# Optimization experiments

Measured on AMD Instinct MI355X. Metric: run time of the kernel, lower is better.

The kernel has to match this reference:

```python
import jax, jax.numpy as jnp
import numpy as np

B, NUM, LENTH, AUX = 32, 64, 64, 64
SIZE, OUT = 256, 256
IN_G = (LENTH + 1) * 2 + AUX  # 194


def _linear_params(k, fan_in, fan_out):
    # torch nn.Linear default init: U(-1/sqrt(fan_in), 1/sqrt(fan_in))
    s = 1.0 / np.sqrt(fan_in)
    kw, kb = jax.random.split(k)
    W = jax.random.uniform(kw, (fan_in, fan_out), minval=-s, maxval=s, dtype=jnp.float32)
    b = jax.random.uniform(kb, (fan_out,), minval=-s, maxval=s, dtype=jnp.float32)
    return W, b


def setup_inputs() -> dict:
    key = jax.random.key(0)
    ks = jax.random.split(key, 8)
    inp = {"x_aux": jax.random.normal(ks[0], (B, NUM, LENTH + AUX), dtype=jnp.float32)}
    dims = [("g1", IN_G, SIZE), ("g2", SIZE, SIZE), ("g3", SIZE, SIZE), ("g4", SIZE, OUT),
            ("f1", OUT, SIZE), ("f2", SIZE, SIZE), ("f3", SIZE, OUT)]
    for k, (name, fi, fo) in zip(ks[1:], dims):
        W, b = _linear_params(k, fi, fo)
        inp[name + "_w"] = W
        inp[name + "_b"] = b
    return inp


def reference(x_aux, g1_w, g1_b, g2_w, g2_b, g3_w, g3_b, g4_w, g4_b,
              f1_w, f1_b, f2_w, f2_b, f3_w, f3_b):
    bsz = x_aux.shape[0]
    # coord feature = object index i
    coord = jnp.broadcast_to(
        jnp.arange(NUM, dtype=x_aux.dtype)[None, :, None], (bsz, NUM, 1))
    x = jnp.concatenate([x_aux[:, :, :LENTH], coord], axis=-1)      # [B, N, LENTH+1]
    xa = jnp.concatenate([x_aux, coord], axis=-1)                   # [B, N, LENTH+AUX+1]
    # all-pairs broadcast+concat -> [B, N, N, IN_G]
    x_i = jnp.broadcast_to(x[:, None, :, :], (bsz, NUM, NUM, LENTH + 1))
    x_j = jnp.broadcast_to(xa[:, :, None, :], (bsz, NUM, NUM, LENTH + AUX + 1))
    pairs = jnp.concatenate([x_i, x_j], axis=-1)
    # shared g-MLP over every pair
    h = jax.nn.relu(pairs @ g1_w + g1_b)
    h = jax.nn.relu(h @ g2_w + g2_b)
    h = jax.nn.relu(h @ g3_w + g3_b)
    h = jax.nn.relu(h @ g4_w + g4_b)
    # sum-pool over all N*N pairs -> [B, OUT]
    x_g = h.sum(axis=(1, 2))
    # f-MLP (dropout treated as identity / eval mode)
    x_f = jax.nn.relu(x_g @ f1_w + f1_b)
    x_f = jax.nn.relu(x_f @ f2_w + f2_b)
    return x_f @ f3_w + f3_b
```

## Files before the change

### kernel.cpp

```cpp
#include <hip/hip_runtime.h>

#define BATCH 32
#define NOBJ  64
#define PADK  264

typedef _Float16 f16x2 __attribute__((ext_vector_type(2)));
typedef _Float16 f16x4 __attribute__((ext_vector_type(4)));
typedef _Float16 f16x8 __attribute__((ext_vector_type(8)));
typedef float    f32x4 __attribute__((ext_vector_type(4)));
typedef float    f32x16 __attribute__((ext_vector_type(16)));

#define MFMA32(a, b, c) __builtin_amdgcn_mfma_f32_32x32x16_f16((a), (b), (c), 0, 0, 0)


__global__ __launch_bounds__(256) void precompute_ci(
    const float* __restrict__ x_aux, const float* __restrict__ g1w,
    float* __restrict__ ci) {
  __shared__ float xs[4][128];
  const int blk = blockIdx.x;
  const int b  = blk >> 4;
  const int i0 = (blk & 15) * 4;
  const int t  = threadIdx.x;

#pragma unroll
  for (int u = 0; u < 2; ++u) {
    int idx = u * 256 + t;
    int j = idx >> 7, k = idx & 127;
    xs[j][k] = x_aux[((size_t)(b * NOBJ + i0 + j)) * 128 + k];
  }
  __syncthreads();

  float c0 = 0.f, c1 = 0.f, c2 = 0.f, c3 = 0.f;
#pragma unroll 8
  for (int k = 0; k < 128; ++k) {
    float w = g1w[(size_t)(65 + k) * 256 + t];
    c0 += xs[0][k] * w; c1 += xs[1][k] * w;
    c2 += xs[2][k] * w; c3 += xs[3][k] * w;
  }
  float wc = g1w[(size_t)193 * 256 + t];
  c0 += (float)(i0 + 0) * wc;
  c1 += (float)(i0 + 1) * wc;
  c2 += (float)(i0 + 2) * wc;
  c3 += (float)(i0 + 3) * wc;
  ci[((size_t)(b * NOBJ + i0 + 0)) * 256 + t] = c0;
  ci[((size_t)(b * NOBJ + i0 + 1)) * 256 + t] = c1;
  ci[((size_t)(b * NOBJ + i0 + 2)) * 256 + t] = c2;
  ci[((size_t)(b * NOBJ + i0 + 3)) * 256 + t] = c3;
}

__global__ __launch_bounds__(256) void prep_weights(
    const float* __restrict__ g1w, const float* __restrict__ g2w,
    const float* __restrict__ g3w, const float* __restrict__ g4w,
    _Float16* __restrict__ wtf, float* __restrict__ xg) {
  __shared__ _Float16 tile[256][33];
  const int blk = blockIdx.x;
  const int t = threadIdx.x;
  xg[blk * 256 + t] = 0.0f;

  const int l  = blk >> 3;
  const int nt = blk & 7;
  const float* src = (l == 0) ? g1w : (l == 1) ? g2w : (l == 2) ? g3w : g4w;

  const int nn = t & 31, kb = t >> 5;
#pragma unroll 4
  for (int pass = 0; pass < 32; ++pass) {
    int kp = pass * 8 + kb;
    int kl;
    if (l == 0) {
      kl = (kp <= 64) ? kp : -1;
    } else {
      kl = 64 * (kp >> 6) + 32 * (kp & 1) + ((kp & 63) >> 1);
    }
    float v = (kl >= 0) ? src[(size_t)kl * 256 + nt * 32 + nn] : 0.0f;
    tile[kp][nn] = (_Float16)v;
  }
  __syncthreads();

  const int lane = t & 63;
  const int nfrag = lane & 31;
  const int kbase = (lane >> 5) * 8;
  _Float16* dst = wtf + ((size_t)(l * 8 + nt) * 16) * 512;
#pragma unroll
  for (int q = 0; q < 4; ++q) {
    int kk = (t >> 6) + 4 * q;
    f16x8 fr;
#pragma unroll
    for (int j = 0; j < 8; ++j)
      fr[j] = tile[kk * 16 + kbase + j][nfrag];
    *(f16x8*)(dst + (size_t)kk * 512 + lane * 8) = fr;
  }
}

template <int STEPS>
__device__ __forceinline__ void do_layer(
    const _Float16* __restrict__ bp0, const _Float16* __restrict__ bp1,
    const _Float16* __restrict__ arow, f32x16 acc[8]) {
  f16x8 b0[STEPS], b1[STEPS];
#pragma unroll
  for (int kk = 0; kk < STEPS; ++kk) {
    b0[kk] = *(const f16x8*)(bp0 + kk * 512);
    b1[kk] = *(const f16x8*)(bp1 + kk * 512);
  }
#pragma unroll
  for (int kk = 0; kk < STEPS; ++kk) {
#pragma unroll
    for (int m = 0; m < 4; ++m) {
      f16x8 a = *(const f16x8*)(arow + (size_t)m * 32 * PADK + kk * 16);
      acc[m * 2]     = MFMA32(a, b0[kk], acc[m * 2]);
      acc[m * 2 + 1] = MFMA32(a, b1[kk], acc[m * 2 + 1]);
    }
  }
}

__global__ __launch_bounds__(256, 2) void g_mlp_pool(
    const float* __restrict__ x_aux,
    const _Float16* __restrict__ wtf,
    const float* __restrict__ ci,
    const float* __restrict__ g1b, const float* __restrict__ g2b,
    const float* __restrict__ g3b, const float* __restrict__ g4b,
    float* __restrict__ xg) {
  __shared__ _Float16 As[128][PADK];

  const int b  = blockIdx.x >> 5;
  const int i0 = (blockIdx.x & 31) * 2;
  const int t  = threadIdx.x;

  {
    const float* xb = x_aux + (size_t)b * NOBJ * 128;
    const int c4 = t & 15, r0 = t >> 4;
#pragma unroll
    for (int it = 0; it < 8; ++it) {
      int r = it * 16 + r0;
      f32x4 v = *(const f32x4*)(xb + (size_t)(r & 63) * 128 + c4 * 4);
      f16x4 hh = {(_Float16)v[0], (_Float16)v[1], (_Float16)v[2], (_Float16)v[3]};
      *(f16x4*)&As[r][c4 * 4] = hh;
    }
    if (t < 128) {
      f16x8 z1 = {};
      z1[0] = (_Float16)(t & 63);
      *(f16x8*)&As[t][64] = z1;
      f16x8 z = {};
      *(f16x8*)&As[t][72] = z;
    }
  }
  __syncthreads();

  const int lane = t & 63;
  const int nq   = t >> 6;
  const int c31  = lane & 31;
  const int h    = lane >> 5;
  const int n0   = nq * 64;
  const float* gb[4] = {g1b, g2b, g3b, g4b};

  const float* cb = ci + (size_t)(b * NOBJ + i0) * 256;
  const float ci_v[2][2] = {{cb[n0 + c31], cb[n0 + 32 + c31]},
                            {cb[256 + n0 + c31], cb[256 + 32 + n0 + c31]}};

  for (int layer = 0; layer < 4; ++layer) {
    const float bv0 = gb[layer][n0 + c31];
    const float bv1 = gb[layer][n0 + 32 + c31];

    f32x16 acc[8];

    const _Float16* bp0 =
        wtf + ((size_t)(layer * 8 + nq * 2) * 16) * 512 + lane * 8;
    const _Float16* bp1 = bp0 + 16 * 512;
    const _Float16* arow = &As[c31][h * 8];

    if (layer == 0) {
#pragma unroll
      for (int m = 0; m < 4; ++m)
#pragma unroll
        for (int ns = 0; ns < 2; ++ns)
#pragma unroll
          for (int reg = 0; reg < 16; ++reg)
            acc[m * 2 + ns][reg] = ci_v[m >> 1][ns];
      do_layer<5>(bp0, bp1, arow, acc);
    } else {
#pragma unroll
      for (int x = 0; x < 8; ++x) acc[x] = (f32x16){};
      do_layer<16>(bp0, bp1, arow, acc);
    }

    if (layer < 3) {
      __syncthreads();
#pragma unroll
      for (int m = 0; m < 4; ++m)
#pragma unroll
        for (int g = 0; g < 4; ++g)
#pragma unroll
          for (int r = 0; r < 4; ++r) {
            const int row = m * 32 + g * 8 + h * 4 + r;
            const int reg = g * 4 + r;
            f16x2 pk = {(_Float16)fmaxf(acc[m * 2][reg] + bv0, 0.f),
                        (_Float16)fmaxf(acc[m * 2 + 1][reg] + bv1, 0.f)};
            *(f16x2*)&As[row][n0 + 2 * c31] = pk;
          }
      __syncthreads();
    } else {
      float s0 = 0.f, s1 = 0.f;
#pragma unroll
      for (int m = 0; m < 4; ++m)
#pragma unroll
        for (int reg = 0; reg < 16; ++reg) {
          s0 += fmaxf(acc[m * 2][reg] + bv0, 0.f);
          s1 += fmaxf(acc[m * 2 + 1][reg] + bv1, 0.f);
        }
      s0 += __shfl_xor(s0, 32, 64);
      s1 += __shfl_xor(s1, 32, 64);
      if (h == 0) {
        atomicAdd(&xg[b * 256 + n0 + c31], s0);
        atomicAdd(&xg[b * 256 + n0 + 32 + c31], s1);
      }
    }
  }
}

__global__ __launch_bounds__(1024) void f_mlp(
    const float* __restrict__ xg,
    const float* __restrict__ f1w, const float* __restrict__ f1b,
    const float* __restrict__ f2w, const float* __restrict__ f2b,
    const float* __restrict__ f3w, const float* __restrict__ f3b,
    float* __restrict__ out) {
  __shared__ float xs[256], ys[256], ps[4][256];
  const int b = blockIdx.x;
  const int t = threadIdx.x;
  const int n = t & 255;
  const int kc = t >> 8;

  if (t < 256) xs[t] = xg[b * 256 + t];
  __syncthreads();

  float p = 0.f;
#pragma unroll 8
  for (int k0 = 0; k0 < 64; ++k0) {
    int k = kc * 64 + k0;
    p += xs[k] * f1w[k * 256 + n];
  }
  ps[kc][n] = p;
  __syncthreads();
  if (t < 256)
    ys[t] = fmaxf(f1b[t] + ps[0][t] + ps[1][t] + ps[2][t] + ps[3][t], 0.f);
  __syncthreads();

  p = 0.f;
#pragma unroll 8
  for (int k0 = 0; k0 < 64; ++k0) {
    int k = kc * 64 + k0;
    p += ys[k] * f2w[k * 256 + n];
  }
  ps[kc][n] = p;
  __syncthreads();
  if (t < 256)
    xs[t] = fmaxf(f2b[t] + ps[0][t] + ps[1][t] + ps[2][t] + ps[3][t], 0.f);
  __syncthreads();

  p = 0.f;
#pragma unroll 8
  for (int k0 = 0; k0 < 64; ++k0) {
    int k = kc * 64 + k0;
    p += xs[k] * f3w[k * 256 + n];
  }
  ps[kc][n] = p;
  __syncthreads();
  if (t < 256)
    out[b * 256 + t] = f3b[t] + ps[0][t] + ps[1][t] + ps[2][t] + ps[3][t];
}

extern "C" void kernel_launch(void* const* d_in, const int* in_sizes, int n_in,
                              void* d_out, int out_size, void* d_ws, size_t ws_size,
                              hipStream_t stream) {
  const float* x_aux = (const float*)d_in[0];
  const float* g1w = (const float*)d_in[1];
  const float* g1b = (const float*)d_in[2];
  const float* g2w = (const float*)d_in[3];
  const float* g2b = (const float*)d_in[4];
  const float* g3w = (const float*)d_in[5];
  const float* g3b = (const float*)d_in[6];
  const float* g4w = (const float*)d_in[7];
  const float* g4b = (const float*)d_in[8];
  const float* f1w = (const float*)d_in[9];
  const float* f1b = (const float*)d_in[10];
  const float* f2w = (const float*)d_in[11];
  const float* f2b = (const float*)d_in[12];
  const float* f3w = (const float*)d_in[13];
  const float* f3b = (const float*)d_in[14];
  float* out = (float*)d_out;

  _Float16* wtf = (_Float16*)d_ws;
  float* xg = (float*)((char*)d_ws + 512u * 1024u);
  float* ci = (float*)((char*)d_ws + 512u * 1024u + 32u * 1024u);

  hipLaunchKernelGGL(precompute_ci, dim3(512), dim3(256), 0, stream,
                     x_aux, g1w, ci);
  hipLaunchKernelGGL(prep_weights, dim3(32), dim3(256), 0, stream,
                     g1w, g2w, g3w, g4w, wtf, xg);
  hipLaunchKernelGGL(g_mlp_pool, dim3(BATCH * 32), dim3(256), 0, stream,
                     x_aux, wtf, ci, g1b, g2b, g3b, g4b, xg);
  hipLaunchKernelGGL(f_mlp, dim3(BATCH), dim3(1024), 0, stream,
                     xg, f1w, f1b, f2w, f2b, f3w, f3b, out);
}
```

Baseline: 163.3 us.

## Merge prep kernels and fuse f-MLP into g-MLP tail via last-block counter

Combines the ci precompute and weight prep into one launch, and removes the separate f_mlp kernel by having the last block per batch (detected with an atomic counter) run the f-MLP. This cuts two kernel launches and their inter-kernel gaps. In exchange, the f-MLP now runs on 256 threads with a full 256-long serial dot product per thread, and correctness depends on fences and the counter being reset every call.

```diff
diff --git a/kernel.cpp b/kernel.cpp
--- a/kernel.cpp
+++ b/kernel.cpp
@@ -13,81 +13,82 @@
 #define MFMA32(a, b, c) __builtin_amdgcn_mfma_f32_32x32x16_f16((a), (b), (c), 0, 0, 0)
 
 
-__global__ __launch_bounds__(256) void precompute_ci(
-    const float* __restrict__ x_aux, const float* __restrict__ g1w,
-    float* __restrict__ ci) {
-  __shared__ float xs[4][128];
-  const int blk = blockIdx.x;
-  const int b  = blk >> 4;
-  const int i0 = (blk & 15) * 4;
-  const int t  = threadIdx.x;
-
-#pragma unroll
-  for (int u = 0; u < 2; ++u) {
-    int idx = u * 256 + t;
-    int j = idx >> 7, k = idx & 127;
-    xs[j][k] = x_aux[((size_t)(b * NOBJ + i0 + j)) * 128 + k];
-  }
-  __syncthreads();
-
-  float c0 = 0.f, c1 = 0.f, c2 = 0.f, c3 = 0.f;
-#pragma unroll 8
-  for (int k = 0; k < 128; ++k) {
-    float w = g1w[(size_t)(65 + k) * 256 + t];
-    c0 += xs[0][k] * w; c1 += xs[1][k] * w;
-    c2 += xs[2][k] * w; c3 += xs[3][k] * w;
-  }
-  float wc = g1w[(size_t)193 * 256 + t];
-  c0 += (float)(i0 + 0) * wc;
-  c1 += (float)(i0 + 1) * wc;
-  c2 += (float)(i0 + 2) * wc;
-  c3 += (float)(i0 + 3) * wc;
-  ci[((size_t)(b * NOBJ + i0 + 0)) * 256 + t] = c0;
-  ci[((size_t)(b * NOBJ + i0 + 1)) * 256 + t] = c1;
-  ci[((size_t)(b * NOBJ + i0 + 2)) * 256 + t] = c2;
-  ci[((size_t)(b * NOBJ + i0 + 3)) * 256 + t] = c3;
-}
-
-__global__ __launch_bounds__(256) void prep_weights(
+__global__ __launch_bounds__(256) void prep_all(
+    const float* __restrict__ x_aux,
     const float* __restrict__ g1w, const float* __restrict__ g2w,
     const float* __restrict__ g3w, const float* __restrict__ g4w,
-    _Float16* __restrict__ wtf, float* __restrict__ xg) {
+    _Float16* __restrict__ wtf, float* __restrict__ xg,
+    float* __restrict__ ci, int* __restrict__ cnt) {
   __shared__ _Float16 tile[256][33];
   const int blk = blockIdx.x;
   const int t = threadIdx.x;
-  xg[blk * 256 + t] = 0.0f;
-
-  const int l  = blk >> 3;
-  const int nt = blk & 7;
-  const float* src = (l == 0) ? g1w : (l == 1) ? g2w : (l == 2) ? g3w : g4w;
-
-  const int nn = t & 31, kb = t >> 5;
+
+  if (blk < 32) {
+    xg[blk * 256 + t] = 0.0f;
+    if (blk == 0 && t < 32) cnt[t] = 0;
+
+    const int l  = blk >> 3;
+    const int nt = blk & 7;
+    const float* src = (l == 0) ? g1w : (l == 1) ? g2w : (l == 2) ? g3w : g4w;
+
+    const int nn = t & 31, kb = t >> 5;
 #pragma unroll 4
-  for (int pass = 0; pass < 32; ++pass) {
-    int kp = pass * 8 + kb;
-    int kl;
-    if (l == 0) {
-      kl = (kp <= 64) ? kp : -1;
-    } else {
-      kl = 64 * (kp >> 6) + 32 * (kp & 1) + ((kp & 63) >> 1);
-    }
-    float v = (kl >= 0) ? src[(size_t)kl * 256 + nt * 32 + nn] : 0.0f;
-    tile[kp][nn] = (_Float16)v;
-  }
-  __syncthreads();
-
-  const int lane = t & 63;
-  const int nfrag = lane & 31;
-  const int kbase = (lane >> 5) * 8;
-  _Float16* dst = wtf + ((size_t)(l * 8 + nt) * 16) * 512;
-#pragma unroll
-  for (int q = 0; q < 4; ++q) {
-    int kk = (t >> 6) + 4 * q;
-    f16x8 fr;
-#pragma unroll
-    for (int j = 0; j < 8; ++j)
-      fr[j] = tile[kk * 16 + kbase + j][nfrag];
-    *(f16x8*)(dst + (size_t)kk * 512 + lane * 8) = fr;
+    for (int pass = 0; pass < 32; ++pass) {
+      int kp = pass * 8 + kb;
+      int kl;
+      if (l == 0) {
+        kl = (kp <= 64) ? kp : -1;
+      } else {
+        kl = 64 * (kp >> 6) + 32 * (kp & 1) + ((kp & 63) >> 1);
+      }
+      float v = (kl >= 0) ? src[(size_t)kl * 256 + nt * 32 + nn] : 0.0f;
+      tile[kp][nn] = (_Float16)v;
+    }
+    __syncthreads();
+
+    const int lane = t & 63;
+    const int nfrag = lane & 31;
+    const int kbase = (lane >> 5) * 8;
+    _Float16* dst = wtf + ((size_t)(l * 8 + nt) * 16) * 512;
+#pragma unroll
+    for (int q = 0; q < 4; ++q) {
+      int kk = (t >> 6) + 4 * q;
+      f16x8 fr;
+#pragma unroll
+      for (int j = 0; j < 8; ++j)
+        fr[j] = tile[kk * 16 + kbase + j][nfrag];
+      *(f16x8*)(dst + (size_t)kk * 512 + lane * 8) = fr;
+    }
+  } else {
+    float* xs = (float*)&tile[0][0];
+    const int blkc = blk - 32;
+    const int b  = blkc >> 4;
+    const int i0 = (blkc & 15) * 4;
+
+#pragma unroll
+    for (int u = 0; u < 2; ++u) {
+      int idx = u * 256 + t;
+      int j = idx >> 7, k = idx & 127;
+      xs[j * 128 + k] = x_aux[((size_t)(b * NOBJ + i0 + j)) * 128 + k];
+    }
+    __syncthreads();
+
+    float c0 = 0.f, c1 = 0.f, c2 = 0.f, c3 = 0.f;
+#pragma unroll 8
+    for (int k = 0; k < 128; ++k) {
+      float w = g1w[(size_t)(65 + k) * 256 + t];
+      c0 += xs[k] * w;       c1 += xs[128 + k] * w;
+      c2 += xs[256 + k] * w; c3 += xs[384 + k] * w;
+    }
+    float wc = g1w[(size_t)193 * 256 + t];
+    c0 += (float)(i0 + 0) * wc;
+    c1 += (float)(i0 + 1) * wc;
+    c2 += (float)(i0 + 2) * wc;
+    c3 += (float)(i0 + 3) * wc;
+    ci[((size_t)(b * NOBJ + i0 + 0)) * 256 + t] = c0;
+    ci[((size_t)(b * NOBJ + i0 + 1)) * 256 + t] = c1;
+    ci[((size_t)(b * NOBJ + i0 + 2)) * 256 + t] = c2;
+    ci[((size_t)(b * NOBJ + i0 + 3)) * 256 + t] = c3;
   }
 }
 
@@ -118,8 +119,14 @@
     const float* __restrict__ ci,
     const float* __restrict__ g1b, const float* __restrict__ g2b,
     const float* __restrict__ g3b, const float* __restrict__ g4b,
-    float* __restrict__ xg) {
+    float* __restrict__ xg,
+    int* __restrict__ cnt,
+    const float* __restrict__ f1w, const float* __restrict__ f1b,
+    const float* __restrict__ f2w, const float* __restrict__ f2b,
+    const float* __restrict__ f3w, const float* __restrict__ f3b,
+    float* __restrict__ out) {
   __shared__ _Float16 As[128][PADK];
+  __shared__ int is_last;
 
   const int b  = blockIdx.x >> 5;
   const int i0 = (blockIdx.x & 31) * 2;
@@ -154,7 +161,7 @@
 
   const float* cb = ci + (size_t)(b * NOBJ + i0) * 256;
   const float ci_v[2][2] = {{cb[n0 + c31], cb[n0 + 32 + c31]},
-                            {cb[256 + n0 + c31], cb[256 + 32 + n0 + c31]}};
+                            {cb[256 + n0 + c31], cb[256 + n0 + 32 + c31]}};
 
   for (int layer = 0; layer < 4; ++layer) {
     const float bv0 = gb[layer][n0 + c31];
@@ -214,57 +221,39 @@
       }
     }
   }
-}
-
-__global__ __launch_bounds__(1024) void f_mlp(
-    const float* __restrict__ xg,
-    const float* __restrict__ f1w, const float* __restrict__ f1b,
-    const float* __restrict__ f2w, const float* __restrict__ f2b,
-    const float* __restrict__ f3w, const float* __restrict__ f3b,
-    float* __restrict__ out) {
-  __shared__ float xs[256], ys[256], ps[4][256];
-  const int b = blockIdx.x;
-  const int t = threadIdx.x;
-  const int n = t & 255;
-  const int kc = t >> 8;
-
-  if (t < 256) xs[t] = xg[b * 256 + t];
-  __syncthreads();
-
-  float p = 0.f;
-#pragma unroll 8
-  for (int k0 = 0; k0 < 64; ++k0) {
-    int k = kc * 64 + k0;
-    p += xs[k] * f1w[k * 256 + n];
-  }
-  ps[kc][n] = p;
-  __syncthreads();
-  if (t < 256)
-    ys[t] = fmaxf(f1b[t] + ps[0][t] + ps[1][t] + ps[2][t] + ps[3][t], 0.f);
-  __syncthreads();
-
-  p = 0.f;
-#pragma unroll 8
-  for (int k0 = 0; k0 < 64; ++k0) {
-    int k = kc * 64 + k0;
-    p += ys[k] * f2w[k * 256 + n];
-  }
-  ps[kc][n] = p;
-  __syncthreads();
-  if (t < 256)
-    xs[t] = fmaxf(f2b[t] + ps[0][t] + ps[1][t] + ps[2][t] + ps[3][t], 0.f);
-  __syncthreads();
-
-  p = 0.f;
-#pragma unroll 8
-  for (int k0 = 0; k0 < 64; ++k0) {
-    int k = kc * 64 + k0;
-    p += xs[k] * f3w[k * 256 + n];
-  }
-  ps[kc][n] = p;
-  __syncthreads();
-  if (t < 256)
-    out[b * 256 + t] = f3b[t] + ps[0][t] + ps[1][t] + ps[2][t] + ps[3][t];
+
+  __syncthreads();
+  if (t == 0) {
+    __threadfence();
+    is_last = (atomicAdd(&cnt[b], 1) == 31) ? 1 : 0;
+  }
+  __syncthreads();
+  if (!is_last) return;
+
+  float* fx = (float*)&As[0][0];
+  float* fy = fx + 256;
+
+  __threadfence();
+  fx[t] = __hip_atomic_load(&xg[b * 256 + t], __ATOMIC_RELAXED,
+                            __HIP_MEMORY_SCOPE_AGENT);
+  __syncthreads();
+
+  float a = f1b[t];
+#pragma unroll 16
+  for (int k = 0; k < 256; ++k) a += fx[k] * f1w[(size_t)k * 256 + t];
+  fy[t] = fmaxf(a, 0.f);
+  __syncthreads();
+
+  a = f2b[t];
+#pragma unroll 16
+  for (int k = 0; k < 256; ++k) a += fy[k] * f2w[(size_t)k * 256 + t];
+  fx[t] = fmaxf(a, 0.f);
+  __syncthreads();
+
+  a = f3b[t];
+#pragma unroll 16
+  for (int k = 0; k < 256; ++k) a += fx[k] * f3w[(size_t)k * 256 + t];
+  out[b * 256 + t] = a;
 }
 
 extern "C" void kernel_launch(void* const* d_in, const int* in_sizes, int n_in,
@@ -290,13 +279,12 @@
   _Float16* wtf = (_Float16*)d_ws;
   float* xg = (float*)((char*)d_ws + 512u * 1024u);
   float* ci = (float*)((char*)d_ws + 512u * 1024u + 32u * 1024u);
-
-  hipLaunchKernelGGL(precompute_ci, dim3(512), dim3(256), 0, stream,
-                     x_aux, g1w, ci);
-  hipLaunchKernelGGL(prep_weights, dim3(32), dim3(256), 0, stream,
-                     g1w, g2w, g3w, g4w, wtf, xg);
+  int* cnt  = (int*)((char*)d_ws + 512u * 1024u + 32u * 1024u
+                     + 2048u * 1024u);
+
+  hipLaunchKernelGGL(prep_all, dim3(544), dim3(256), 0, stream,
+                     x_aux, g1w, g2w, g3w, g4w, wtf, xg, ci, cnt);
   hipLaunchKernelGGL(g_mlp_pool, dim3(BATCH * 32), dim3(256), 0, stream,
-                     x_aux, wtf, ci, g1b, g2b, g3b, g4b, xg);
-  hipLaunchKernelGGL(f_mlp, dim3(BATCH), dim3(1024), 0, stream,
-                     xg, f1w, f1b, f2w, f2b, f3w, f3b, out);
-}
+                     x_aux, wtf, ci, g1b, g2b, g3b, g4b, xg, cnt,
+                     f1w, f1b, f2w, f2b, f3w, f3b, out);
+}
```

Measured after the change: 201.3 us. +23.3%, slower.

## Decompose first g-layer into per-object terms and merge prep kernels

Applied to the files above, without the earlier changes.

The first g-MLP layer is split into two parts: one term depends only on j and one only on i plus bias. Both are precomputed per object in a merged prep kernel. The main kernel then builds layer-1 activations as relu(h0j + ci) in shared memory instead of running a K=80 MFMA layer over every pair, and the two prep launches become one 800-block launch. This removes a quarter of the per-pair GEMM work and one launch. In exchange it writes and reads extra fp32 intermediate buffers in workspace.

```diff
diff --git a/kernel.cpp b/kernel.cpp
--- a/kernel.cpp
+++ b/kernel.cpp
@@ -13,96 +13,117 @@
 #define MFMA32(a, b, c) __builtin_amdgcn_mfma_f32_32x32x16_f16((a), (b), (c), 0, 0, 0)
 
 
-__global__ __launch_bounds__(256) void precompute_ci(
-    const float* __restrict__ x_aux, const float* __restrict__ g1w,
-    float* __restrict__ ci) {
-  __shared__ float xs[4][128];
-  const int blk = blockIdx.x;
-  const int b  = blk >> 4;
-  const int i0 = (blk & 15) * 4;
-  const int t  = threadIdx.x;
-
-#pragma unroll
-  for (int u = 0; u < 2; ++u) {
-    int idx = u * 256 + t;
-    int j = idx >> 7, k = idx & 127;
-    xs[j][k] = x_aux[((size_t)(b * NOBJ + i0 + j)) * 128 + k];
-  }
-  __syncthreads();
-
-  float c0 = 0.f, c1 = 0.f, c2 = 0.f, c3 = 0.f;
-#pragma unroll 8
-  for (int k = 0; k < 128; ++k) {
-    float w = g1w[(size_t)(65 + k) * 256 + t];
-    c0 += xs[0][k] * w; c1 += xs[1][k] * w;
-    c2 += xs[2][k] * w; c3 += xs[3][k] * w;
-  }
-  float wc = g1w[(size_t)193 * 256 + t];
-  c0 += (float)(i0 + 0) * wc;
-  c1 += (float)(i0 + 1) * wc;
-  c2 += (float)(i0 + 2) * wc;
-  c3 += (float)(i0 + 3) * wc;
-  ci[((size_t)(b * NOBJ + i0 + 0)) * 256 + t] = c0;
-  ci[((size_t)(b * NOBJ + i0 + 1)) * 256 + t] = c1;
-  ci[((size_t)(b * NOBJ + i0 + 2)) * 256 + t] = c2;
-  ci[((size_t)(b * NOBJ + i0 + 3)) * 256 + t] = c3;
-}
-
-__global__ __launch_bounds__(256) void prep_weights(
-    const float* __restrict__ g1w, const float* __restrict__ g2w,
-    const float* __restrict__ g3w, const float* __restrict__ g4w,
-    _Float16* __restrict__ wtf, float* __restrict__ xg) {
+__global__ __launch_bounds__(256) void prep_all(
+    const float* __restrict__ x_aux,
+    const float* __restrict__ g1w, const float* __restrict__ g1b,
+    const float* __restrict__ g2w, const float* __restrict__ g3w,
+    const float* __restrict__ g4w,
+    _Float16* __restrict__ wtf, float* __restrict__ xg,
+    float* __restrict__ cib, float* __restrict__ h0j) {
   __shared__ _Float16 tile[256][33];
   const int blk = blockIdx.x;
   const int t = threadIdx.x;
-  xg[blk * 256 + t] = 0.0f;
-
-  const int l  = blk >> 3;
-  const int nt = blk & 7;
-  const float* src = (l == 0) ? g1w : (l == 1) ? g2w : (l == 2) ? g3w : g4w;
-
-  const int nn = t & 31, kb = t >> 5;
+
+  if (blk < 32) {
+    xg[blk * 256 + t] = 0.0f;
+    const int l = blk >> 3;
+    if (l == 0) return;
+    const int nt = blk & 7;
+    const float* src = (l == 1) ? g2w : (l == 2) ? g3w : g4w;
+
+    const int nn = t & 31, kb = t >> 5;
 #pragma unroll 4
-  for (int pass = 0; pass < 32; ++pass) {
-    int kp = pass * 8 + kb;
-    int kl;
-    if (l == 0) {
-      kl = (kp <= 64) ? kp : -1;
-    } else {
-      kl = 64 * (kp >> 6) + 32 * (kp & 1) + ((kp & 63) >> 1);
-    }
-    float v = (kl >= 0) ? src[(size_t)kl * 256 + nt * 32 + nn] : 0.0f;
-    tile[kp][nn] = (_Float16)v;
-  }
-  __syncthreads();
-
-  const int lane = t & 63;
-  const int nfrag = lane & 31;
-  const int kbase = (lane >> 5) * 8;
-  _Float16* dst = wtf + ((size_t)(l * 8 + nt) * 16) * 512;
-#pragma unroll
-  for (int q = 0; q < 4; ++q) {
-    int kk = (t >> 6) + 4 * q;
-    f16x8 fr;
-#pragma unroll
-    for (int j = 0; j < 8; ++j)
-      fr[j] = tile[kk * 16 + kbase + j][nfrag];
-    *(f16x8*)(dst + (size_t)kk * 512 + lane * 8) = fr;
-  }
-}
-
-template <int STEPS>
-__device__ __forceinline__ void do_layer(
+    for (int pass = 0; pass < 32; ++pass) {
+      int kp = pass * 8 + kb;
+      int kl = (l == 1) ? kp
+                        : 64 * (kp >> 6) + 32 * (kp & 1) + ((kp & 63) >> 1);
+      tile[kp][nn] = (_Float16)src[(size_t)kl * 256 + nt * 32 + nn];
+    }
+    __syncthreads();
+
+    const int lane = t & 63;
+    const int nfrag = lane & 31;
+    const int kbase = (lane >> 5) * 8;
+    _Float16* dst = wtf + ((size_t)(l * 8 + nt) * 16) * 512;
+#pragma unroll
+    for (int q = 0; q < 4; ++q) {
+      int kk = (t >> 6) + 4 * q;
+      f16x8 fr;
+#pragma unroll
+      for (int j = 0; j < 8; ++j)
+        fr[j] = tile[kk * 16 + kbase + j][nfrag];
+      *(f16x8*)(dst + (size_t)kk * 512 + lane * 8) = fr;
+    }
+  } else if (blk < 544) {
+    float* xs = (float*)&tile[0][0];
+    const int blkc = blk - 32;
+    const int b  = blkc >> 4;
+    const int i0 = (blkc & 15) * 4;
+
+#pragma unroll
+    for (int u = 0; u < 2; ++u) {
+      int idx = u * 256 + t;
+      int j = idx >> 7, k = idx & 127;
+      xs[j * 128 + k] = x_aux[((size_t)(b * NOBJ + i0 + j)) * 128 + k];
+    }
+    __syncthreads();
+
+    float c0 = 0.f, c1 = 0.f, c2 = 0.f, c3 = 0.f;
+#pragma unroll 8
+    for (int k = 0; k < 128; ++k) {
+      float w = g1w[(size_t)(65 + k) * 256 + t];
+      c0 += xs[k] * w;       c1 += xs[128 + k] * w;
+      c2 += xs[256 + k] * w; c3 += xs[384 + k] * w;
+    }
+    float wc = g1w[(size_t)193 * 256 + t];
+    float bb = g1b[t];
+    c0 += (float)(i0 + 0) * wc + bb;
+    c1 += (float)(i0 + 1) * wc + bb;
+    c2 += (float)(i0 + 2) * wc + bb;
+    c3 += (float)(i0 + 3) * wc + bb;
+    cib[((size_t)(b * NOBJ + i0 + 0)) * 256 + t] = c0;
+    cib[((size_t)(b * NOBJ + i0 + 1)) * 256 + t] = c1;
+    cib[((size_t)(b * NOBJ + i0 + 2)) * 256 + t] = c2;
+    cib[((size_t)(b * NOBJ + i0 + 3)) * 256 + t] = c3;
+  } else {
+    float* xs = (float*)&tile[0][0];
+    const int blk2 = blk - 544;
+    const int b  = blk2 >> 3;
+    const int j0 = (blk2 & 7) * 8;
+
+#pragma unroll
+    for (int u = 0; u < 2; ++u) {
+      int idx = u * 256 + t;
+      int jj = idx >> 6, k = idx & 63;
+      xs[jj * 65 + k] = x_aux[((size_t)(b * NOBJ + j0 + jj)) * 128 + k];
+    }
+    if (t < 8) xs[t * 65 + 64] = (float)(j0 + t);
+    __syncthreads();
+
+    float acc[8] = {};
+#pragma unroll 5
+    for (int k = 0; k < 65; ++k) {
+      float w = g1w[(size_t)k * 256 + t];
+#pragma unroll
+      for (int jj = 0; jj < 8; ++jj) acc[jj] += xs[jj * 65 + k] * w;
+    }
+#pragma unroll
+    for (int jj = 0; jj < 8; ++jj)
+      h0j[((size_t)(b * NOBJ + j0 + jj)) * 256 + t] = acc[jj];
+  }
+}
+
+__device__ __forceinline__ void do_layer16(
     const _Float16* __restrict__ bp0, const _Float16* __restrict__ bp1,
     const _Float16* __restrict__ arow, f32x16 acc[8]) {
-  f16x8 b0[STEPS], b1[STEPS];
-#pragma unroll
-  for (int kk = 0; kk < STEPS; ++kk) {
+  f16x8 b0[16], b1[16];
+#pragma unroll
+  for (int kk = 0; kk < 16; ++kk) {
     b0[kk] = *(const f16x8*)(bp0 + kk * 512);
     b1[kk] = *(const f16x8*)(bp1 + kk * 512);
   }
 #pragma unroll
-  for (int kk = 0; kk < STEPS; ++kk) {
+  for (int kk = 0; kk < 16; ++kk) {
 #pragma unroll
     for (int m = 0; m < 4; ++m) {
       f16x8 a = *(const f16x8*)(arow + (size_t)m * 32 * PADK + kk * 16);
@@ -113,74 +134,62 @@
 }
 
 __global__ __launch_bounds__(256, 2) void g_mlp_pool(
-    const float* __restrict__ x_aux,
+    const float* __restrict__ h0j,
+    const float* __restrict__ cib,
     const _Float16* __restrict__ wtf,
-    const float* __restrict__ ci,
-    const float* __restrict__ g1b, const float* __restrict__ g2b,
-    const float* __restrict__ g3b, const float* __restrict__ g4b,
+    const float* __restrict__ g2b, const float* __restrict__ g3b,
+    const float* __restrict__ g4b,
     float* __restrict__ xg) {
   __shared__ _Float16 As[128][PADK];
 
   const int b  = blockIdx.x >> 5;
   const int i0 = (blockIdx.x & 31) * 2;
   const int t  = threadIdx.x;
+  const int lane = t & 63;
+  const int wv   = t >> 6;
 
   {
-    const float* xb = x_aux + (size_t)b * NOBJ * 128;
-    const int c4 = t & 15, r0 = t >> 4;
-#pragma unroll
-    for (int it = 0; it < 8; ++it) {
-      int r = it * 16 + r0;
-      f32x4 v = *(const f32x4*)(xb + (size_t)(r & 63) * 128 + c4 * 4);
-      f16x4 hh = {(_Float16)v[0], (_Float16)v[1], (_Float16)v[2], (_Float16)v[3]};
-      *(f16x4*)&As[r][c4 * 4] = hh;
-    }
-    if (t < 128) {
-      f16x8 z1 = {};
-      z1[0] = (_Float16)(t & 63);
-      *(f16x8*)&As[t][64] = z1;
-      f16x8 z = {};
-      *(f16x8*)&As[t][72] = z;
-    }
-  }
-  __syncthreads();
-
-  const int lane = t & 63;
-  const int nq   = t >> 6;
+    const int c = lane * 4;
+    const float* hb = h0j + (size_t)(b * NOBJ) * 256 + c;
+    const float* c0p = cib + (size_t)(b * NOBJ + i0) * 256 + c;
+    f32x4 cv0 = *(const f32x4*)c0p;
+    f32x4 cv1 = *(const f32x4*)(c0p + 256);
+#pragma unroll
+    for (int it = 0; it < 16; ++it) {
+      int j = it * 4 + wv;
+      f32x4 hv = *(const f32x4*)(hb + (size_t)j * 256);
+      f16x4 p0, p1;
+#pragma unroll
+      for (int q = 0; q < 4; ++q) {
+        p0[q] = (_Float16)fmaxf(hv[q] + cv0[q], 0.f);
+        p1[q] = (_Float16)fmaxf(hv[q] + cv1[q], 0.f);
+      }
+      *(f16x4*)&As[j][c]      = p0;
+      *(f16x4*)&As[64 + j][c] = p1;
+    }
+  }
+  __syncthreads();
+
+  const int nq   = wv;
   const int c31  = lane & 31;
   const int h    = lane >> 5;
   const int n0   = nq * 64;
-  const float* gb[4] = {g1b, g2b, g3b, g4b};
-
-  const float* cb = ci + (size_t)(b * NOBJ + i0) * 256;
-  const float ci_v[2][2] = {{cb[n0 + c31], cb[n0 + 32 + c31]},
-                            {cb[256 + n0 + c31], cb[256 + 32 + n0 + c31]}};
-
-  for (int layer = 0; layer < 4; ++layer) {
+  const float* gb[4] = {nullptr, g2b, g3b, g4b};
+
+  for (int layer = 1; layer < 4; ++layer) {
     const float bv0 = gb[layer][n0 + c31];
     const float bv1 = gb[layer][n0 + 32 + c31];
 
     f32x16 acc[8];
+#pragma unroll
+    for (int x = 0; x < 8; ++x) acc[x] = (f32x16){};
 
     const _Float16* bp0 =
         wtf + ((size_t)(layer * 8 + nq * 2) * 16) * 512 + lane * 8;
     const _Float16* bp1 = bp0 + 16 * 512;
     const _Float16* arow = &As[c31][h * 8];
 
-    if (layer == 0) {
-#pragma unroll
-      for (int m = 0; m < 4; ++m)
-#pragma unroll
-        for (int ns = 0; ns < 2; ++ns)
-#pragma unroll
-          for (int reg = 0; reg < 16; ++reg)
-            acc[m * 2 + ns][reg] = ci_v[m >> 1][ns];
-      do_layer<5>(bp0, bp1, arow, acc);
-    } else {
-#pragma unroll
-      for (int x = 0; x < 8; ++x) acc[x] = (f32x16){};
-      do_layer<16>(bp0, bp1, arow, acc);
-    }
+    do_layer16(bp0, bp1, arow, acc);
 
     if (layer < 3) {
       __syncthreads();
@@ -288,15 +297,14 @@
   float* out = (float*)d_out;
 
   _Float16* wtf = (_Float16*)d_ws;
-  float* xg = (float*)((char*)d_ws + 512u * 1024u);
-  float* ci = (float*)((char*)d_ws + 512u * 1024u + 32u * 1024u);
-
-  hipLaunchKernelGGL(precompute_ci, dim3(512), dim3(256), 0, stream,
-                     x_aux, g1w, ci);
-  hipLaunchKernelGGL(prep_weights, dim3(32), dim3(256), 0, stream,
-                     g1w, g2w, g3w, g4w, wtf, xg);
+  float* xg  = (float*)((char*)d_ws + 512u * 1024u);
+  float* cib = (float*)((char*)d_ws + 544u * 1024u);
+  float* h0j = (float*)((char*)d_ws + 544u * 1024u + 2048u * 1024u);
+
+  hipLaunchKernelGGL(prep_all, dim3(800), dim3(256), 0, stream,
+                     x_aux, g1w, g1b, g2w, g3w, g4w, wtf, xg, cib, h0j);
   hipLaunchKernelGGL(g_mlp_pool, dim3(BATCH * 32), dim3(256), 0, stream,
-                     x_aux, wtf, ci, g1b, g2b, g3b, g4b, xg);
+                     h0j, cib, wtf, g2b, g3b, g4b, xg);
   hipLaunchKernelGGL(f_mlp, dim3(BATCH), dim3(1024), 0, stream,
                      xg, f1w, f1b, f2w, f2b, f3w, f3b, out);
 }
```

Measured after the change: 147.6 us. 9.6% less time.
